# Optimization experiments

Measured on AMD Instinct MI355X. Metric: run time of the kernel, lower is better.

Reference implementation:

```python
import jax, jax.numpy as jnp
import numpy as np
from jax import lax

N = 256        # graph nodes (== conv5 channels)
C = 128        # diff-pool clusters
E = 4096       # number of edges
EPS = 1e-15    # PyG dense_diff_pool entropy eps


def setup_inputs():
    key = jax.random.key(0)
    ks = jax.random.split(key, 24)
    def rn(k, shape, scale):
        return jax.random.normal(k, shape, dtype=jnp.float32) * scale
    inp = {
        "inputs": jax.random.normal(ks[0], (1, 3, 512, 512), dtype=jnp.float32),
        "edge_index": jax.random.randint(ks[1], (2, E), 0, N, dtype=jnp.int32),
    }
    convs = [(3, 32), (32, 64), (64, 128), (128, 256), (256, 256)]
    for i, (ci, co) in enumerate(convs):
        inp[f"w{i+1}"] = rn(ks[2 + i], (co, ci, 3, 3), 0.05)
        inp[f"b{i+1}"] = jnp.zeros((co,), jnp.float32)
    sages = [(256, 2), (256, 128), (2, 2)]
    for i, (ci, co) in enumerate(sages):
        inp[f"s{i+1}_wl"] = rn(ks[10 + 3 * i], (ci, co), 0.1)
        inp[f"s{i+1}_wr"] = rn(ks[11 + 3 * i], (ci, co), 0.1)
        inp[f"s{i+1}_b"] = jnp.zeros((co,), jnp.float32)
    return inp


def _conv_block(x, w, b):
    # 3x3 SAME conv -> relu -> 2x2 max pool (stride 2), NCHW layout
    x = lax.conv_general_dilated(x, w, (1, 1), 'SAME',
                                 dimension_numbers=('NCHW', 'OIHW', 'NCHW'))
    x = jax.nn.relu(x + b[None, :, None, None])
    return lax.reduce_window(x, -jnp.inf, lax.max,
                             (1, 1, 2, 2), (1, 1, 2, 2), 'VALID')


def _sage(x, src, dst, wl, wr, b, n):
    # PyG SAGEConv(normalize=False): lin_l(mean_{src->dst} x_src) + lin_r(x)
    tot = jax.ops.segment_sum(x[src], dst, num_segments=n)
    cnt = jax.ops.segment_sum(jnp.ones((dst.shape[0],), x.dtype), dst, num_segments=n)
    agg = jnp.where(cnt[:, None] > 0, tot / jnp.maximum(cnt, 1.0)[:, None], 0.0)
    return agg @ wl + b + x @ wr


def reference(inputs, edge_index, w1, b1, w2, b2, w3, b3, w4, b4, w5, b5,
              s1_wl, s1_wr, s1_b, s2_wl, s2_wr, s2_b, s3_wl, s3_wr, s3_b):
    x = inputs
    for w, b in ((w1, b1), (w2, b2), (w3, b3), (w4, b4), (w5, b5)):
        x = _conv_block(x, w, b)
    org = x.reshape(N, N)  # (256 channels, 16*16 spatial) -> node features
    src, dst = edge_index[0], edge_index[1]
    x1 = _sage(org, src, dst, s1_wl, s1_wr, s1_b, N)  # (256, 2)
    s = _sage(org, src, dst, s2_wl, s2_wr, s2_b, N)   # (256, 128)
    # dense adjacency (duplicate edges accumulate, matching scipy coo.todense())
    adj = jnp.zeros((N, N), org.dtype).at[src, dst].add(1.0)
    # dense_diff_pool
    s_soft = jax.nn.softmax(s, axis=-1)
    x_pool = s_soft.T @ x1               # (128, 2)
    adj_pool = s_soft.T @ adj @ s_soft   # (128, 128)
    link_loss = jnp.linalg.norm(adj - s_soft @ s_soft.T) / (N * N)
    ent_loss = (-s_soft * jnp.log(s_soft + EPS)).sum(-1).mean()
    nodes = jnp.tanh(x_pool)             # (128, 2)
    # per-row argmax-equality thresholding (vectorized: rows are independent)
    row_max = adj_pool.max(axis=1, keepdims=True)
    edge_bin = (adj_pool == row_max).astype(org.dtype)  # (128, 128)
    # sage3 over the binarized dense adjacency (equivalent to dense_to_sparse + SAGEConv)
    indeg = edge_bin.sum(axis=0)
    agg = jnp.where(indeg[:, None] > 0,
                    (edge_bin.T @ nodes) / jnp.maximum(indeg, 1.0)[:, None], 0.0)
    out = agg @ s3_wl + s3_b + nodes @ s3_wr  # (128, 2)
    return out.reshape(-1), link_loss, ent_loss, nodes, edge_bin
```

## Files before the change

kernel.cpp:

```cpp
#include <hip/hip_runtime.h>
#include <math.h>

#define NN 256
#define NE 4096
#define NC 128

using short8  = __attribute__((ext_vector_type(8))) short;
using short4v = __attribute__((ext_vector_type(4))) short;
using f32x4   = __attribute__((ext_vector_type(4))) float;

static __device__ __forceinline__ unsigned short f2bf(float x) {
    unsigned u = __float_as_uint(x);
    unsigned r = (u + 0x7FFF + ((u >> 16) & 1)) >> 16;
    return (unsigned short)r;
}

static __device__ __forceinline__ float block_sum_256(float v, float* red4) {
    #pragma unroll
    for (int o = 32; o > 0; o >>= 1) v += __shfl_xor(v, o);
    __syncthreads();
    if ((threadIdx.x & 63) == 0) red4[threadIdx.x >> 6] = v;
    __syncthreads();
    return (red4[0] + red4[1]) + (red4[2] + red4[3]);
}

__global__ void wfrag_prep_all(const float* __restrict__ w1, const float* __restrict__ w2,
                               const float* __restrict__ w3, const float* __restrict__ w4,
                               const float* __restrict__ w5,
                               unsigned short* __restrict__ f1, unsigned short* __restrict__ f2,
                               unsigned short* __restrict__ f3, unsigned short* __restrict__ f4,
                               unsigned short* __restrict__ f5)
{
    int b = blockIdx.x;
    if (b == 477) {
        int idx = threadIdx.x;
        int lane = idx & 63, rest = idx >> 6;
        int g = rest & 1, slot = rest >> 1;
        int oc = g * 16 + (lane & 15);
        short8 v;
        #pragma unroll
        for (int j = 0; j < 8; ++j) {
            int k = (lane >> 4) * 8 + j;
            float wv = 0.f;
            if (slot == 0) {
                int tap = k >> 2, ch = k & 3;
                if (ch < 3) wv = w1[oc * 27 + ch * 9 + tap];
            } else {
                if (k < 3) wv = w1[oc * 27 + k * 9 + 8];
            }
            v[j] = (short)f2bf(wv);
        }
        *(short8*)&f1[(size_t)idx * 8] = v;
        return;
    }
    const float* w; unsigned short* f; int CIN, NG, NCH, base;
    if (b < 9)        { w = w2; f = f2; CIN = 32;  NG = 4;  NCH = 1; base = 0;   }
    else if (b < 45)  { w = w3; f = f3; CIN = 64;  NG = 8;  NCH = 2; base = 9;   }
    else if (b < 189) { w = w4; f = f4; CIN = 128; NG = 16; NCH = 4; base = 45;  }
    else              { w = w5; f = f5; CIN = 256; NG = 16; NCH = 8; base = 189; }
    int idx = (b - base) * 256 + threadIdx.x;
    int lane = idx & 63, rest = idx >> 6;
    int c = rest % NCH; rest /= NCH;
    int g = rest % NG;  int t = rest / NG;
    if (t >= 9) return;
    int oc = g * 16 + (lane & 15);
    int cin0 = c * 32 + (lane >> 4) * 8;
    short8 v;
    #pragma unroll
    for (int j = 0; j < 8; ++j) {
        v[j] = (short)f2bf(w[((size_t)oc * CIN + cin0 + j) * 9 + t]);
    }
    *(short8*)&f[(size_t)idx * 8] = v;
}

__global__ __launch_bounds__(256) void conv1_mfma(
    const float* __restrict__ in, const unsigned short* __restrict__ wf1,
    const float* __restrict__ bias, unsigned short* __restrict__ out)
{
    constexpr int Hc = 512, TR = 8;
    const int tid = threadIdx.x;
    const int lane = tid & 63, wid = tid >> 6;
    const int col = lane & 15, kgl = lane >> 4;
    const int X0 = blockIdx.x * 16, Y0 = blockIdx.y * TR;
    __shared__ __align__(16) unsigned short lds[10][18][4];
    if (tid < 180) {
        int hy = tid / 18, hx = tid - hy * 18;
        int gy = Y0 + hy - 1, gx = X0 + hx - 1;
        float v0 = 0.f, v1 = 0.f, v2 = 0.f;
        if (gy >= 0 && gy < Hc && gx >= 0 && gx < Hc) {
            v0 = in[0 * 262144 + gy * 512 + gx];
            v1 = in[1 * 262144 + gy * 512 + gx];
            v2 = in[2 * 262144 + gy * 512 + gx];
        }
        uint2 uu;
        uu.x = f2bf(v0) | ((unsigned)f2bf(v1) << 16);
        uu.y = f2bf(v2);
        *(uint2*)&lds[hy][hx][0] = uu;
    }
    short8 af[2][2];
    #pragma unroll
    for (int slot = 0; slot < 2; ++slot) {
        #pragma unroll
        for (int g = 0; g < 2; ++g) {
            af[slot][g] = *(const short8*)&wf1[((size_t)((slot * 2 + g) * 64 + lane)) * 8];
        }
    }
    __syncthreads();
    f32x4 acc[2][2];
    #pragma unroll
    for (int g = 0; g < 2; ++g) {
        #pragma unroll
        for (int r = 0; r < 2; ++r) acc[g][r] = {0.f, 0.f, 0.f, 0.f};
    }
    const int t0 = 2 * kgl, t1 = 2 * kgl + 1;
    const int dy0 = t0 / 3, dx0 = t0 % 3, dy1 = t1 / 3, dx1 = t1 % 3;
    #pragma unroll
    for (int r = 0; r < 2; ++r) {
        const int py = wid * 2 + r;
        short4v lo = *(const short4v*)&lds[py + dy0][col + dx0][0];
        short4v hi = *(const short4v*)&lds[py + dy1][col + dx1][0];
        short8 bf0 = __builtin_shufflevector(lo, hi, 0, 1, 2, 3, 4, 5, 6, 7);
        short4v z4 = {0, 0, 0, 0};
        short4v t8 = z4;
        if (kgl == 0) t8 = *(const short4v*)&lds[py + 2][col + 2][0];
        short8 bf1 = __builtin_shufflevector(t8, z4, 0, 1, 2, 3, 4, 5, 6, 7);
        #pragma unroll
        for (int g = 0; g < 2; ++g) {
            acc[g][r] = __builtin_amdgcn_mfma_f32_16x16x32_bf16(af[0][g], bf0, acc[g][r], 0, 0, 0);
            acc[g][r] = __builtin_amdgcn_mfma_f32_16x16x32_bf16(af[1][g], bf1, acc[g][r], 0, 0, 0);
        }
    }
    #pragma unroll
    for (int g = 0; g < 2; ++g) {
        const int oc = g * 16 + kgl * 4;
        const float4 bb = *(const float4*)&bias[oc];
        const float bbv[4] = {bb.x, bb.y, bb.z, bb.w};
        float vv[4];
        #pragma unroll
        for (int q = 0; q < 4; ++q) {
            float v = fmaxf(acc[g][0][q], acc[g][1][q]);
            v = fmaxf(v, __shfl_xor(v, 1));
            vv[q] = fmaxf(v + bbv[q], 0.f);
        }
        if (!(col & 1)) {
            unsigned u0 = f2bf(vv[0]) | ((unsigned)f2bf(vv[1]) << 16);
            unsigned u1 = f2bf(vv[2]) | ((unsigned)f2bf(vv[3]) << 16);
            const int pry = Y0 / 2 + wid;
            const int prx = X0 / 2 + (col >> 1);
            uint2 uu; uu.x = u0; uu.y = u1;
            *(uint2*)&out[((size_t)(pry * 256 + prx)) * 32 + oc] = uu;
        }
    }
}

template<int CIN, int COUT, int Hc, int OCB, int CSPLIT>
__global__ __launch_bounds__(256) void conv_mfma(
    const unsigned short* __restrict__ in, const unsigned short* __restrict__ wfrag,
    const float* __restrict__ bias, void* __restrict__ outv)
{
    constexpr int TR = 8;
    constexpr int NOG = OCB / 16;
    constexpr int NG  = COUT / 16;
    constexpr int NCHT = CIN / 32;
    constexpr int NCH = NCHT / CSPLIT;
    constexpr int RPW = TR / 4;
    const int tid = threadIdx.x;
    const int lane = tid & 63, wid = tid >> 6;
    const int col = lane & 15, kgl = lane >> 4;
    const int X0 = blockIdx.x * 16, Y0 = blockIdx.y * TR;
    const int ob = blockIdx.z / CSPLIT, cs = blockIdx.z % CSPLIT;

    __shared__ __align__(16) unsigned short lds[(TR + 2) * 4 * 18 * 8];

    f32x4 acc[NOG][RPW];
    #pragma unroll
    for (int g = 0; g < NOG; ++g) {
        #pragma unroll
        for (int r = 0; r < RPW; ++r) acc[g][r] = {0.f, 0.f, 0.f, 0.f};
    }

    for (int cc = 0; cc < NCH; ++cc) {
        const int ca = cs * NCH + cc;
        __syncthreads();
        constexpr int ITEMS = (TR + 2) * 18 * 4;
        for (int i = tid; i < ITEMS; i += 256) {
            int kg = i & 3, rem = i >> 2;
            int hx = rem % 18, hy = rem / 18;
            int gy = Y0 + hy - 1, gx = X0 + hx - 1;
            short8 v = {0, 0, 0, 0, 0, 0, 0, 0};
            if (gy >= 0 && gy < Hc && gx >= 0 && gx < Hc) {
                v = *(const short8*)&in[((size_t)(gy * Hc + gx)) * CIN + ca * 32 + kg * 8];
            }
            *(short8*)&lds[((hy * 4 + kg) * 18 + hx) * 8] = v;
        }
        __syncthreads();
        #pragma unroll
        for (int t = 0; t < 9; ++t) {
            const int ky = t / 3, kx = t % 3;
            short8 af[NOG];
            #pragma unroll
            for (int g = 0; g < NOG; ++g) {
                af[g] = *(const short8*)&wfrag[((((size_t)t * NG + ob * NOG + g) * NCHT + ca) * 64 + lane) * 8];
            }
            #pragma unroll
            for (int r = 0; r < RPW; ++r) {
                const int py = wid * RPW + r;
                short8 bf = *(const short8*)&lds[(((py + ky) * 4 + kgl) * 18 + col + kx) * 8];
                #pragma unroll
                for (int g = 0; g < NOG; ++g) {
                    acc[g][r] = __builtin_amdgcn_mfma_f32_16x16x32_bf16(af[g], bf, acc[g][r], 0, 0, 0);
                }
            }
        }
    }

    if constexpr (CSPLIT == 1) {
        constexpr int Wp = Hc / 2;
        unsigned short* outp = (unsigned short*)outv;
        #pragma unroll
        for (int g = 0; g < NOG; ++g) {
            const int oc = (ob * NOG + g) * 16 + kgl * 4;
            const float4 bb = *(const float4*)&bias[oc];
            const float bbv[4] = {bb.x, bb.y, bb.z, bb.w};
            #pragma unroll
            for (int pr = 0; pr < RPW / 2; ++pr) {
                float vv[4];
                #pragma unroll
                for (int q = 0; q < 4; ++q) {
                    float v = fmaxf(acc[g][2 * pr][q], acc[g][2 * pr + 1][q]);
                    v = fmaxf(v, __shfl_xor(v, 1));
                    vv[q] = fmaxf(v + bbv[q], 0.f);
                }
                if (!(col & 1)) {
                    unsigned u0 = f2bf(vv[0]) | ((unsigned)f2bf(vv[1]) << 16);
                    unsigned u1 = f2bf(vv[2]) | ((unsigned)f2bf(vv[3]) << 16);
                    const int pry = Y0 / 2 + wid * (RPW / 2) + pr;
                    const int prx = X0 / 2 + (col >> 1);
                    uint2 uu; uu.x = u0; uu.y = u1;
                    *(uint2*)&outp[((size_t)(pry * Wp + prx)) * COUT + oc] = uu;
                }
            }
        }
    } else {
        float* po = (float*)outv;
        #pragma unroll
        for (int g = 0; g < NOG; ++g) {
            #pragma unroll
            for (int r = 0; r < RPW; ++r) {
                const int gy = Y0 + wid * RPW + r;
                #pragma unroll
                for (int q = 0; q < 4; ++q) {
                    const int oc = (ob * NOG + g) * 16 + kgl * 4 + q;
                    po[((size_t)(cs * COUT + oc) * Hc + gy) * Hc + X0 + col] = acc[g][r][q];
                }
            }
        }
    }
}

template<int COUT, int HP, int CS>
__global__ void finalize_pool(const float* __restrict__ partial, const float* __restrict__ bias,
                              float* __restrict__ out)
{
    int idx = blockIdx.x * 256 + threadIdx.x;
    if (idx >= COUT * HP * HP) return;
    constexpr int H = HP * 2;
    int x = idx & (HP - 1); int rest = idx / HP;
    int y = rest & (HP - 1); int oc = rest / HP;
    float v00 = 0.f, v01 = 0.f, v10 = 0.f, v11 = 0.f;
    #pragma unroll
    for (int cs = 0; cs < CS; ++cs) {
        const float* p = partial + ((size_t)(cs * COUT + oc) * H + 2 * y) * H + 2 * x;
        v00 += p[0]; v01 += p[1]; v10 += p[H]; v11 += p[H + 1];
    }
    float m = fmaxf(fmaxf(v00, v01), fmaxf(v10, v11)) + bias[oc];
    out[idx] = fmaxf(m, 0.f);
}


__global__ void zero_kernel(float* p) { p[blockIdx.x * 256 + threadIdx.x] = 0.f; }

__global__ void adj_build_kernel(const int* __restrict__ src, const int* __restrict__ dst,
                                 float* adj, float* adjT)
{
    int e = blockIdx.x * 256 + threadIdx.x;
    int s = src[e], d = dst[e];
    atomicAdd(&adj[s * NN + d], 1.0f);
    atomicAdd(&adjT[d * NN + s], 1.0f);
}

__global__ __launch_bounds__(256) void node_fused_kernel(
    const float* __restrict__ adjT, const float* __restrict__ org,
    const float* __restrict__ s1wl, const float* __restrict__ s1wr, const float* __restrict__ s1b,
    const float* __restrict__ s2wl, const float* __restrict__ s2wr, const float* __restrict__ s2b,
    float* __restrict__ s_soft, float* __restrict__ s_softT,
    float* __restrict__ x1g, float* __restrict__ entp)
{
    int n = blockIdx.x, t = threadIdx.x;
    __shared__ float rowT[256], orgn[256], aggn[256], red[256], sm[128], red4[4];
    float rT = adjT[n * 256 + t];
    rowT[t] = rT; orgn[t] = org[n * 256 + t];
    __syncthreads();
    float cnt = block_sum_256(rT, red4);
    float a0 = 0.f, a1 = 0.f, a2 = 0.f, a3 = 0.f;
    #pragma unroll 8
    for (int s = 0; s < 256; s += 4) {
        a0 = fmaf(rowT[s + 0], org[(s + 0) * 256 + t], a0);
        a1 = fmaf(rowT[s + 1], org[(s + 1) * 256 + t], a1);
        a2 = fmaf(rowT[s + 2], org[(s + 2) * 256 + t], a2);
        a3 = fmaf(rowT[s + 3], org[(s + 3) * 256 + t], a3);
    }
    float acc = (a0 + a1) + (a2 + a3);
    float aggv = (cnt > 0.f) ? acc / cnt : 0.f;
    aggn[t] = aggv;
    float orgv = orgn[t];
    float x10 = block_sum_256(aggv * s1wl[2 * t] + orgv * s1wr[2 * t], red4) + s1b[0];
    float x11 = block_sum_256(aggv * s1wl[2 * t + 1] + orgv * s1wr[2 * t + 1], red4) + s1b[1];
    if (t == 0) { x1g[n * 2 + 0] = x10; x1g[n * 2 + 1] = x11; }
    int p = t & 127, h = t >> 7;
    float b0 = 0.f, b1 = 0.f, b2 = 0.f, b3 = 0.f;
    #pragma unroll 8
    for (int k = h * 128; k < h * 128 + 128; k += 2) {
        b0 = fmaf(aggn[k],     s2wl[k * NC + p],       b0);
        b1 = fmaf(orgn[k],     s2wr[k * NC + p],       b1);
        b2 = fmaf(aggn[k + 1], s2wl[(k + 1) * NC + p], b2);
        b3 = fmaf(orgn[k + 1], s2wr[(k + 1) * NC + p], b3);
    }
    red[t] = (b0 + b1) + (b2 + b3);
    __syncthreads();
    if (t < 128) sm[p] = red[t] + red[t + 128] + s2b[p];
    __syncthreads();
    if (t < 128) red[t] = sm[t];
    __syncthreads();
    for (int s = 64; s > 0; s >>= 1) { if (t < s) red[t] = fmaxf(red[t], red[t + s]); __syncthreads(); }
    float mx = red[0];
    __syncthreads();
    float e = 0.f;
    if (t < 128) { e = expf(sm[t] - mx); red[t] = e; } else { red[t] = 0.f; }
    __syncthreads();
    for (int s = 64; s > 0; s >>= 1) { if (t < s) red[t] += red[t + s]; __syncthreads(); }
    float denom = red[0];
    float q = e / denom;
    if (t < 128) {
        s_soft[n * NC + t] = q;
        s_softT[t * 256 + n] = q;
    }
    float ev = (t < 128) ? -q * logf(q + 1e-15f) : 0.f;
    float esum = block_sum_256(ev, red4);
    if (t == 0) entp[n] = esum;
}

__global__ __launch_bounds__(256) void row_fused_kernel(
    const float* __restrict__ adj, const float* __restrict__ s_soft,
    const float* __restrict__ s_softT, float* __restrict__ T, float* __restrict__ lpart)
{
    int i = blockIdx.x, j = threadIdx.x;
    __shared__ float si[NC], adjrow[256], tbuf[256], red4[4];
    adjrow[j] = adj[i * 256 + j];
    if (j < NC) si[j] = s_soft[i * NC + j];
    __syncthreads();
    float d0 = 0.f, d1 = 0.f, d2 = 0.f, d3 = 0.f;
    #pragma unroll 8
    for (int k = 0; k < NC; k += 4) {
        d0 = fmaf(si[k + 0], s_softT[(k + 0) * 256 + j], d0);
        d1 = fmaf(si[k + 1], s_softT[(k + 1) * 256 + j], d1);
        d2 = fmaf(si[k + 2], s_softT[(k + 2) * 256 + j], d2);
        d3 = fmaf(si[k + 3], s_softT[(k + 3) * 256 + j], d3);
    }
    float dot = (d0 + d1) + (d2 + d3);
    float dd = adjrow[j] - dot;
    float lsum = block_sum_256(dd * dd, red4);
    if (j == 0) lpart[i] = lsum;
    int p = j & 127, h = j >> 7;
    float a0 = 0.f, a1 = 0.f;
    #pragma unroll 8
    for (int k = h * 128; k < h * 128 + 128; k += 2) {
        a0 = fmaf(adjrow[k],     s_soft[k * NC + p],       a0);
        a1 = fmaf(adjrow[k + 1], s_soft[(k + 1) * NC + p], a1);
    }
    tbuf[j] = a0 + a1;
    __syncthreads();
    if (j < 128) T[i * NC + j] = tbuf[j] + tbuf[j + 128];
}

__global__ __launch_bounds__(256) void cluster_fused_kernel(
    const float* __restrict__ s_softT, const float* __restrict__ T, const float* __restrict__ x1g,
    float* __restrict__ eb_out, float* __restrict__ nodes_out)
{
    int c = blockIdx.x, t = threadIdx.x;
    __shared__ float colc[256], red[256], ap[NC], red4[4];
    colc[t] = s_softT[c * 256 + t];
    __syncthreads();
    int p = t & 127, h = t >> 7;
    float a0 = 0.f, a1 = 0.f;
    #pragma unroll 8
    for (int n = h * 128; n < h * 128 + 128; n += 2) {
        a0 = fmaf(colc[n],     T[n * NC + p],       a0);
        a1 = fmaf(colc[n + 1], T[(n + 1) * NC + p], a1);
    }
    red[t] = a0 + a1;
    __syncthreads();
    if (t < 128) ap[t] = red[t] + red[t + 128];
    __syncthreads();
    if (t < 128) red[t] = ap[t];
    __syncthreads();
    for (int s = 64; s > 0; s >>= 1) { if (t < s) red[t] = fmaxf(red[t], red[t + s]); __syncthreads(); }
    float mx = red[0];
    if (t < 128) eb_out[c * NC + t] = (ap[t] == mx) ? 1.f : 0.f;
    float n0 = tanhf(block_sum_256(colc[t] * x1g[t * 2 + 0], red4));
    float n1 = tanhf(block_sum_256(colc[t] * x1g[t * 2 + 1], red4));
    if (t == 0) { nodes_out[c * 2 + 0] = n0; nodes_out[c * 2 + 1] = n1; }
}

__global__ __launch_bounds__(256) void final_kernel(
    const float* __restrict__ lpart, const float* __restrict__ entp,
    const float* __restrict__ eb, const float* __restrict__ nodes,
    const float* __restrict__ wl, const float* __restrict__ wr, const float* __restrict__ b,
    float* __restrict__ out_main, float* __restrict__ out_link, float* __restrict__ out_ent)
{
    int t = threadIdx.x;
    __shared__ float red4[4];
    float ls = block_sum_256(lpart[t], red4);
    if (t == 0) out_link[0] = sqrtf(ls) / (float)(NN * NN);
    float es = block_sum_256(entp[t], red4);
    if (t == 0) out_ent[0] = es / (float)NN;
    if (t < NC) {
        int j = t;
        float i0 = 0.f, i1 = 0.f, a00 = 0.f, a01 = 0.f, a10 = 0.f, a11 = 0.f;
        #pragma unroll 8
        for (int i2 = 0; i2 < NC; i2 += 2) {
            float e0 = eb[i2 * NC + j];
            float e1 = eb[(i2 + 1) * NC + j];
            i0 += e0; i1 += e1;
            a00 = fmaf(e0, nodes[i2 * 2 + 0], a00);
            a01 = fmaf(e0, nodes[i2 * 2 + 1], a01);
            a10 = fmaf(e1, nodes[(i2 + 1) * 2 + 0], a10);
            a11 = fmaf(e1, nodes[(i2 + 1) * 2 + 1], a11);
        }
        float indeg = i0 + i1;
        float a0 = a00 + a10, a1 = a01 + a11;
        float inv = (indeg > 0.f) ? 1.f / fmaxf(indeg, 1.f) : 0.f;
        float g0 = a0 * inv, g1 = a1 * inv;
        float n0 = nodes[j * 2 + 0], n1 = nodes[j * 2 + 1];
        out_main[j * 2 + 0] = g0 * wl[0] + g1 * wl[2] + b[0] + n0 * wr[0] + n1 * wr[2];
        out_main[j * 2 + 1] = g0 * wl[1] + g1 * wl[3] + b[1] + n0 * wr[1] + n1 * wr[3];
    }
}

extern "C" void kernel_launch(void* const* d_in, const int* in_sizes, int n_in,
                              void* d_out, int out_size, void* d_ws, size_t ws_size,
                              hipStream_t stream)
{
    const float* input = (const float*)d_in[0];
    const int* eidx = (const int*)d_in[1];
    const int* src = eidx;
    const int* dst = eidx + NE;
    const float* w1 = (const float*)d_in[2];  const float* b1 = (const float*)d_in[3];
    const float* w2 = (const float*)d_in[4];  const float* b2 = (const float*)d_in[5];
    const float* w3 = (const float*)d_in[6];  const float* b3 = (const float*)d_in[7];
    const float* w4 = (const float*)d_in[8];  const float* b4 = (const float*)d_in[9];
    const float* w5 = (const float*)d_in[10]; const float* b5 = (const float*)d_in[11];
    const float* s1_wl = (const float*)d_in[12]; const float* s1_wr = (const float*)d_in[13];
    const float* s1_b  = (const float*)d_in[14];
    const float* s2_wl = (const float*)d_in[15]; const float* s2_wr = (const float*)d_in[16];
    const float* s2_b  = (const float*)d_in[17];
    const float* s3_wl = (const float*)d_in[18]; const float* s3_wr = (const float*)d_in[19];
    const float* s3_b  = (const float*)d_in[20];

    float* ws = (float*)d_ws;
    unsigned short* c1 = (unsigned short*)(ws);
    unsigned short* c2 = (unsigned short*)(ws + 1048576);
    unsigned short* c3 = (unsigned short*)(ws);
    unsigned short* c4 = (unsigned short*)(ws + 1048576);
    float* P5  = ws;
    float* ORG = ws + 1179648;
    unsigned short* f1 = (unsigned short*)(ws + 1572864);
    unsigned short* f2 = (unsigned short*)(ws + 1573888);
    unsigned short* f3 = (unsigned short*)(ws + 1583104);
    unsigned short* f4 = (unsigned short*)(ws + 1619968);
    unsigned short* f5 = (unsigned short*)(ws + 1767424);
    float* adj     = ws + 2062336;
    float* adjT    = ws + 2127872;
    float* s_soft  = ws + 2193408;
    float* T       = ws + 2226176;
    float* x1g     = ws + 2258944;
    float* lpart   = ws + 2259456;
    float* entp    = ws + 2259712;
    float* s_softT = ws + 2259968;

    float* fout = (float*)d_out;
    float* out_main  = fout;
    float* out_link  = fout + 256;
    float* out_ent   = fout + 257;
    float* out_nodes = fout + 258;
    float* out_eb    = fout + 514;

    wfrag_prep_all<<<478, 256, 0, stream>>>(w1, w2, w3, w4, w5, f1, f2, f3, f4, f5);
    zero_kernel<<<512, 256, 0, stream>>>(adj);
    adj_build_kernel<<<16, 256, 0, stream>>>(src, dst, adj, adjT);

    conv1_mfma<<<dim3(32, 64), 256, 0, stream>>>(input, f1, b1, c1);
    conv_mfma<32,  64, 256, 64, 1><<<dim3(16, 32, 1), 256, 0, stream>>>(c1, f2, b2, c2);
    conv_mfma<64, 128, 128, 64, 1><<<dim3(8, 16, 2),  256, 0, stream>>>(c2, f3, b3, c3);
    conv_mfma<128, 256, 64, 32, 1><<<dim3(4, 8, 8),   256, 0, stream>>>(c3, f4, b4, c4);
    conv_mfma<256, 256, 32, 32, 4><<<dim3(2, 4, 32),  256, 0, stream>>>(c4, f5, b5, P5);
    finalize_pool<256, 16, 4><<<256, 256, 0, stream>>>(P5, b5, ORG);

    node_fused_kernel<<<256, 256, 0, stream>>>(adjT, ORG, s1_wl, s1_wr, s1_b,
                                               s2_wl, s2_wr, s2_b, s_soft, s_softT, x1g, entp);
    row_fused_kernel<<<256, 256, 0, stream>>>(adj, s_soft, s_softT, T, lpart);
    cluster_fused_kernel<<<128, 256, 0, stream>>>(s_softT, T, x1g, out_eb, out_nodes);
    final_kernel<<<1, 256, 0, stream>>>(lpart, entp, out_eb, out_nodes,
                                        s3_wl, s3_wr, s3_b, out_main, out_link, out_ent);
}
```

Measured before the change: 111.8 us.

## Double-buffer conv LDS staging and fold adjacency zero/build into other kernels

The conv_mfma halo staging now uses two LDS buffers. The next channel chunk is loaded into registers while MFMAs run on the current one, which drops one barrier per iteration. Separately, the adjacency zeroing is merged into the weight-prep kernel as extra blocks, and the edge scatter runs as extra blocks of the conv1 kernel, removing two launches. This costs more LDS and registers, and it depends on ordering that the launch sequence provides (zeroing finishes before conv1's atomics).

Result: faster. 101.2 us (-9.5%).

```diff
diff --git a/kernel.cpp b/kernel.cpp
--- a/kernel.cpp
+++ b/kernel.cpp
@@ -24,14 +24,18 @@
     return (red4[0] + red4[1]) + (red4[2] + red4[3]);
 }
 
-__global__ void wfrag_prep_all(const float* __restrict__ w1, const float* __restrict__ w2,
+__global__ void wfrag_zero_all(const float* __restrict__ w1, const float* __restrict__ w2,
                                const float* __restrict__ w3, const float* __restrict__ w4,
                                const float* __restrict__ w5,
                                unsigned short* __restrict__ f1, unsigned short* __restrict__ f2,
                                unsigned short* __restrict__ f3, unsigned short* __restrict__ f4,
-                               unsigned short* __restrict__ f5)
+                               unsigned short* __restrict__ f5, float* __restrict__ adjz)
 {
     int b = blockIdx.x;
+    if (b >= 478) {
+        adjz[(b - 478) * 256 + threadIdx.x] = 0.f;
+        return;
+    }
     if (b == 477) {
         int idx = threadIdx.x;
         int lane = idx & 63, rest = idx >> 6;
@@ -73,15 +77,25 @@
     *(short8*)&f[(size_t)idx * 8] = v;
 }
 
-__global__ __launch_bounds__(256) void conv1_mfma(
+__global__ __launch_bounds__(256) void conv1_adj_kernel(
     const float* __restrict__ in, const unsigned short* __restrict__ wf1,
-    const float* __restrict__ bias, unsigned short* __restrict__ out)
-{
-    constexpr int Hc = 512, TR = 8;
+    const float* __restrict__ bias, unsigned short* __restrict__ out,
+    const int* __restrict__ src, const int* __restrict__ dst,
+    float* __restrict__ adj, float* __restrict__ adjT)
+{
+    const int bid = blockIdx.x;
     const int tid = threadIdx.x;
+    if (bid >= 2048) {
+        int e = (bid - 2048) * 256 + tid;
+        int s = src[e], d = dst[e];
+        atomicAdd(&adj[s * NN + d], 1.0f);
+        atomicAdd(&adjT[d * NN + s], 1.0f);
+        return;
+    }
+    constexpr int Hc = 512;
     const int lane = tid & 63, wid = tid >> 6;
     const int col = lane & 15, kgl = lane >> 4;
-    const int X0 = blockIdx.x * 16, Y0 = blockIdx.y * TR;
+    const int X0 = (bid & 31) * 16, Y0 = (bid >> 5) * 8;
     __shared__ __align__(16) unsigned short lds[10][18][4];
     if (tid < 180) {
         int hy = tid / 18, hx = tid - hy * 18;
@@ -163,14 +177,43 @@
     constexpr int NG  = COUT / 16;
     constexpr int NCHT = CIN / 32;
     constexpr int NCH = NCHT / CSPLIT;
-    constexpr int RPW = TR / 4;
+    constexpr int RPW = 2;
+    constexpr int ITEMS = (TR + 2) * 18 * 4;
+    constexpr int NIT = 3;
     const int tid = threadIdx.x;
     const int lane = tid & 63, wid = tid >> 6;
     const int col = lane & 15, kgl = lane >> 4;
     const int X0 = blockIdx.x * 16, Y0 = blockIdx.y * TR;
     const int ob = blockIdx.z / CSPLIT, cs = blockIdx.z % CSPLIT;
 
-    __shared__ __align__(16) unsigned short lds[(TR + 2) * 4 * 18 * 8];
+    __shared__ __align__(16) unsigned short lds[2][ITEMS * 8];
+
+    int ioff[NIT]; bool ival[NIT]; int loff[NIT];
+    #pragma unroll
+    for (int it = 0; it < NIT; ++it) {
+        int i = tid + it * 256;
+        int kg = i & 3, rem = i >> 2;
+        int hx = rem % 18, hy = rem / 18;
+        int gy = Y0 + hy - 1, gx = X0 + hx - 1;
+        ival[it] = (i < ITEMS) && gy >= 0 && gy < Hc && gx >= 0 && gx < Hc;
+        ioff[it] = (gy * Hc + gx) * CIN + kg * 8;
+        loff[it] = ((hy * 4 + kg) * 18 + hx) * 8;
+    }
+    short8 sreg[NIT];
+    auto sload = [&](int ca) {
+        #pragma unroll
+        for (int it = 0; it < NIT; ++it) {
+            short8 v = {0, 0, 0, 0, 0, 0, 0, 0};
+            if (ival[it]) v = *(const short8*)&in[ioff[it] + ca * 32];
+            sreg[it] = v;
+        }
+    };
+    auto swrite = [&](int buf) {
+        #pragma unroll
+        for (int it = 0; it < NIT; ++it) {
+            if (tid + it * 256 < ITEMS) *(short8*)&lds[buf][loff[it]] = sreg[it];
+        }
+    };
 
     f32x4 acc[NOG][RPW];
     #pragma unroll
@@ -179,21 +222,13 @@
         for (int r = 0; r < RPW; ++r) acc[g][r] = {0.f, 0.f, 0.f, 0.f};
     }
 
+    sload(cs * NCH);
+    swrite(0);
+    __syncthreads();
     for (int cc = 0; cc < NCH; ++cc) {
         const int ca = cs * NCH + cc;
-        __syncthreads();
-        constexpr int ITEMS = (TR + 2) * 18 * 4;
-        for (int i = tid; i < ITEMS; i += 256) {
-            int kg = i & 3, rem = i >> 2;
-            int hx = rem % 18, hy = rem / 18;
-            int gy = Y0 + hy - 1, gx = X0 + hx - 1;
-            short8 v = {0, 0, 0, 0, 0, 0, 0, 0};
-            if (gy >= 0 && gy < Hc && gx >= 0 && gx < Hc) {
-                v = *(const short8*)&in[((size_t)(gy * Hc + gx)) * CIN + ca * 32 + kg * 8];
-            }
-            *(short8*)&lds[((hy * 4 + kg) * 18 + hx) * 8] = v;
-        }
-        __syncthreads();
+        if (cc + 1 < NCH) sload(ca + 1);
+        const unsigned short* L = &lds[cc & 1][0];
         #pragma unroll
         for (int t = 0; t < 9; ++t) {
             const int ky = t / 3, kx = t % 3;
@@ -205,13 +240,14 @@
             #pragma unroll
             for (int r = 0; r < RPW; ++r) {
                 const int py = wid * RPW + r;
-                short8 bf = *(const short8*)&lds[(((py + ky) * 4 + kgl) * 18 + col + kx) * 8];
+                short8 bf = *(const short8*)&L[(((py + ky) * 4 + kgl) * 18 + col + kx) * 8];
                 #pragma unroll
                 for (int g = 0; g < NOG; ++g) {
                     acc[g][r] = __builtin_amdgcn_mfma_f32_16x16x32_bf16(af[g], bf, acc[g][r], 0, 0, 0);
                 }
             }
         }
+        if (cc + 1 < NCH) { swrite((cc + 1) & 1); __syncthreads(); }
     }
 
     if constexpr (CSPLIT == 1) {
@@ -222,23 +258,20 @@
             const int oc = (ob * NOG + g) * 16 + kgl * 4;
             const float4 bb = *(const float4*)&bias[oc];
             const float bbv[4] = {bb.x, bb.y, bb.z, bb.w};
+            float vv[4];
             #pragma unroll
-            for (int pr = 0; pr < RPW / 2; ++pr) {
-                float vv[4];
-                #pragma unroll
-                for (int q = 0; q < 4; ++q) {
-                    float v = fmaxf(acc[g][2 * pr][q], acc[g][2 * pr + 1][q]);
-                    v = fmaxf(v, __shfl_xor(v, 1));
-                    vv[q] = fmaxf(v + bbv[q], 0.f);
-                }
-                if (!(col & 1)) {
-                    unsigned u0 = f2bf(vv[0]) | ((unsigned)f2bf(vv[1]) << 16);
-                    unsigned u1 = f2bf(vv[2]) | ((unsigned)f2bf(vv[3]) << 16);
-                    const int pry = Y0 / 2 + wid * (RPW / 2) + pr;
-                    const int prx = X0 / 2 + (col >> 1);
-                    uint2 uu; uu.x = u0; uu.y = u1;
-                    *(uint2*)&outp[((size_t)(pry * Wp + prx)) * COUT + oc] = uu;
-                }
+            for (int q = 0; q < 4; ++q) {
+                float v = fmaxf(acc[g][0][q], acc[g][1][q]);
+                v = fmaxf(v, __shfl_xor(v, 1));
+                vv[q] = fmaxf(v + bbv[q], 0.f);
+            }
+            if (!(col & 1)) {
+                unsigned u0 = f2bf(vv[0]) | ((unsigned)f2bf(vv[1]) << 16);
+                unsigned u1 = f2bf(vv[2]) | ((unsigned)f2bf(vv[3]) << 16);
+                const int pry = Y0 / 2 + wid;
+                const int prx = X0 / 2 + (col >> 1);
+                uint2 uu; uu.x = u0; uu.y = u1;
+                *(uint2*)&outp[((size_t)(pry * Wp + prx)) * COUT + oc] = uu;
             }
         }
     } else {
@@ -277,17 +310,6 @@
     out[idx] = fmaxf(m, 0.f);
 }
 
-
-__global__ void zero_kernel(float* p) { p[blockIdx.x * 256 + threadIdx.x] = 0.f; }
-
-__global__ void adj_build_kernel(const int* __restrict__ src, const int* __restrict__ dst,
-                                 float* adj, float* adjT)
-{
-    int e = blockIdx.x * 256 + threadIdx.x;
-    int s = src[e], d = dst[e];
-    atomicAdd(&adj[s * NN + d], 1.0f);
-    atomicAdd(&adjT[d * NN + s], 1.0f);
-}
 
 __global__ __launch_bounds__(256) void node_fused_kernel(
     const float* __restrict__ adjT, const float* __restrict__ org,
@@ -495,11 +517,8 @@
     float* out_nodes = fout + 258;
     float* out_eb    = fout + 514;
 
-    wfrag_prep_all<<<478, 256, 0, stream>>>(w1, w2, w3, w4, w5, f1, f2, f3, f4, f5);
-    zero_kernel<<<512, 256, 0, stream>>>(adj);
-    adj_build_kernel<<<16, 256, 0, stream>>>(src, dst, adj, adjT);
-
-    conv1_mfma<<<dim3(32, 64), 256, 0, stream>>>(input, f1, b1, c1);
+    wfrag_zero_all<<<990, 256, 0, stream>>>(w1, w2, w3, w4, w5, f1, f2, f3, f4, f5, adj);
+    conv1_adj_kernel<<<2064, 256, 0, stream>>>(input, f1, b1, c1, src, dst, adj, adjT);
     conv_mfma<32,  64, 256, 64, 1><<<dim3(16, 32, 1), 256, 0, stream>>>(c1, f2, b2, c2);
     conv_mfma<64, 128, 128, 64, 1><<<dim3(8, 16, 2),  256, 0, stream>>>(c2, f3, b3, c3);
     conv_mfma<128, 256, 64, 32, 1><<<dim3(4, 8, 8),   256, 0, stream>>>(c3, f4, b4, c4);
```
